# Kernel optimization log

Hardware: AMD Instinct MI355X
Metric: run time of the kernel (lower is better)

The kernel has to match this reference:

```python
import jax, jax.numpy as jnp
import numpy as np

SIZE = 48          # grid edge
DIST = 4           # local neighborhood edge
PAD = DIST // 2    # padding = 2
PADDED = SIZE + 2 * PAD  # 52
RATE = 5           # recurrent steps
CONVEY = 0.9
N_IN = 2048        # input injection sites


def setup_inputs() -> dict:
    key = jax.random.key(0)
    ks = jax.random.split(key, 8)
    neuron_matrix = jnp.zeros((PADDED, PADDED, PADDED), dtype=jnp.float32)
    vinput = jax.random.normal(ks[0], (N_IN,), dtype=jnp.float32)
    # scale synapse so the 5-step relu recurrence stays numerically tame
    synapse = jax.random.normal(ks[1], (SIZE, SIZE, SIZE, DIST, DIST, DIST), dtype=jnp.float32) * 0.05
    W1 = jax.random.normal(ks[2], (SIZE ** 3, 1024), dtype=jnp.float32) * (1.0 / np.sqrt(SIZE ** 3))
    b1 = jnp.zeros((1024,), dtype=jnp.float32)
    W2 = jax.random.normal(ks[3], (1024, 128), dtype=jnp.float32) * (1.0 / np.sqrt(1024))
    b2 = jnp.zeros((128,), dtype=jnp.float32)
    W3 = jax.random.normal(ks[4], (128, 10), dtype=jnp.float32) * (1.0 / np.sqrt(128))
    b3 = jnp.zeros((10,), dtype=jnp.float32)
    node_idx = jax.random.randint(ks[5], (N_IN, 3), 0, SIZE)  # interior coords
    return {"neuron_matrix": neuron_matrix, "vinput": vinput, "synapse": synapse,
            "W1": W1, "b1": b1, "W2": W2, "b2": b2, "W3": W3, "b3": b3,
            "node_idx": node_idx}


def _windows(p):
    # p: [PADDED]^3 -> sliding DxDxD windows at every interior site: [S,S,S,D,D,D]
    idx = jnp.arange(SIZE)[:, None] + jnp.arange(DIST)[None, :]  # [S, D]
    w = jnp.take(p, idx, axis=0)   # [S, D, P, P]
    w = jnp.take(w, idx, axis=2)   # [S, D, S, D, P]
    w = jnp.take(w, idx, axis=4)   # [S, D, S, D, S, D]
    return jnp.transpose(w, (0, 2, 4, 1, 3, 5))  # [S, S, S, D, D, D]


def reference(neuron_matrix, vinput, synapse, W1, b1, W2, b2, W3, b3, node_idx):
    # inject inputs at (possibly colliding) interior nodes (scatter-add, like +=)
    nm = neuron_matrix.at[node_idx[:, 0] + PAD,
                          node_idx[:, 1] + PAD,
                          node_idx[:, 2] + PAD].add(vinput)
    # recurrent locally-connected 3D neighbor aggregation, RATE steps
    for _ in range(RATE):
        win = _windows(nm)  # [S,S,S,D,D,D]
        agg = jnp.einsum('xyzabc,xyzabc->xyz', synapse, win)  # per-site unique-weight reduce
        interior = jax.nn.relu(agg) * CONVEY
        nm = jnp.pad(interior, PAD)  # re-pad with zeros for next step
    x = interior.reshape(1, SIZE ** 3)
    x = jax.nn.relu(x @ W1 + b1)
    x = jax.nn.relu(x @ W2 + b2)
    return x @ W3 + b3  # [1, 10]
```

## Files before the change

### kernel.cpp

```cpp
#include <hip/hip_runtime.h>

#define S 48
#define D 4
#define PADC 2
#define P 52
#define SITES (S * S * S)
#define PADVOL (P * P * P)
#define N_IN 2048
#define H1 1024
#define H2 128
#define OUTN 10
#define RP 64
#define NCH (SITES / RP)
#define RG 16
#define CHPG (NCH / RG)
#define G2B 32

__global__ void scatter_k(const float* __restrict__ vin,
                          const int* __restrict__ idx,
                          float* __restrict__ nm) {
    int t = blockIdx.x * blockDim.x + threadIdx.x;
    if (t < N_IN) {
        int x = idx[t * 3 + 0] + PADC;
        int y = idx[t * 3 + 1] + PADC;
        int z = idx[t * 3 + 2] + PADC;
        atomicAdd(&nm[(x * P + y) * P + z], vin[t]);
    }
}

__global__ __launch_bounds__(256) void step_k(const float* __restrict__ src,
                                              const float* __restrict__ syn,
                                              float* __restrict__ dst) {
    int tid = threadIdx.x;
    int half = tid & 1;
    int sl = tid >> 1;
    int s = blockIdx.x * 128 + sl;
    int z = s % S;
    int q = s / S;
    int y = q % S;
    int x = q / S;
    const float4* sv = (const float4*)(syn + (size_t)s * 64) + half * 8;
    int a0 = half * 2;
    float acc = 0.0f;
#pragma unroll
    for (int a = 0; a < 2; a++) {
#pragma unroll
        for (int b = 0; b < D; b++) {
            const float* row = src + ((x + a0 + a) * P + (y + b)) * P + z;
            float4 w = sv[a * 4 + b];
            acc += w.x * row[0] + w.y * row[1] + w.z * row[2] + w.w * row[3];
        }
    }
    acc += __shfl_xor(acc, 1);
    if (half == 0) {
        acc = fmaxf(acc, 0.0f) * 0.9f;
        dst[((x + PADC) * P + (y + PADC)) * P + (z + PADC)] = acc;
    }
}

__global__ __launch_bounds__(256) void gemv1_k(const float* __restrict__ nmfin,
                                               const float* __restrict__ W1,
                                               float* __restrict__ partial) {
    __shared__ float xs[RP];
    int t = threadIdx.x;
    int lane = t & 63;
    int i0 = blockIdx.x * RP;

    int i = i0 + lane;
    int z = i % S;
    int q = i / S;
    int y = q % S;
    int x = q / S;
    float v = nmfin[((x + PADC) * P + (y + PADC)) * P + (z + PADC)];
    unsigned long long mask = __ballot(v != 0.0f);
    if (t < RP) xs[t] = v;
    __syncthreads();

    const float4* W4 = (const float4*)W1;
    size_t base = (size_t)i0 * (H1 / 4) + t;
    float4 a0 = {0.f, 0.f, 0.f, 0.f};
    float4 a1 = {0.f, 0.f, 0.f, 0.f};
    while (mask) {
        int r0 = (int)__builtin_ctzll(mask);
        mask &= mask - 1;
        if (mask) {
            int r1 = (int)__builtin_ctzll(mask);
            mask &= mask - 1;
            float x0 = xs[r0], x1 = xs[r1];
            float4 w0 = W4[base + (size_t)r0 * (H1 / 4)];
            float4 w1 = W4[base + (size_t)r1 * (H1 / 4)];
            a0.x += x0 * w0.x; a0.y += x0 * w0.y; a0.z += x0 * w0.z; a0.w += x0 * w0.w;
            a1.x += x1 * w1.x; a1.y += x1 * w1.y; a1.z += x1 * w1.z; a1.w += x1 * w1.w;
        } else {
            float x0 = xs[r0];
            float4 w0 = W4[base + (size_t)r0 * (H1 / 4)];
            a0.x += x0 * w0.x; a0.y += x0 * w0.y; a0.z += x0 * w0.z; a0.w += x0 * w0.w;
        }
    }
    float4 acc = {a0.x + a1.x, a0.y + a1.y, a0.z + a1.z, a0.w + a1.w};
    ((float4*)(partial + (size_t)blockIdx.x * H1))[t] = acc;
}

__global__ __launch_bounds__(256) void reduceA_k(const float* __restrict__ partial,
                                                 float* __restrict__ redB) {
    int g = blockIdx.x >> 2;
    int c = (blockIdx.x & 3) * 256 + threadIdx.x;
    float s = 0.0f;
    int r0 = g * CHPG;
#pragma unroll 4
    for (int r = r0; r < r0 + CHPG; r++) s += partial[(size_t)r * H1 + c];
    redB[g * H1 + c] = s;
}

__global__ __launch_bounds__(128) void gemv2_k(const float* __restrict__ redB,
                                               const float* __restrict__ b1,
                                               const float* __restrict__ W2,
                                               float* __restrict__ partial2) {
    __shared__ float ys[H1 / G2B];
    int b = blockIdx.x;
    int t = threadIdx.x;
    int r0 = b * (H1 / G2B);
    if (t < H1 / G2B) {
        int j = r0 + t;
        float s = b1[j];
#pragma unroll
        for (int g = 0; g < RG; g++) s += redB[g * H1 + j];
        ys[t] = fmaxf(s, 0.0f);
    }
    __syncthreads();
    float acc = 0.0f;
#pragma unroll
    for (int i = 0; i < H1 / G2B; i++)
        acc += ys[i] * W2[(size_t)(r0 + i) * H2 + t];
    partial2[b * H2 + t] = acc;
}

__global__ __launch_bounds__(128) void final_k(const float* __restrict__ partial2,
                                               const float* __restrict__ b2,
                                               const float* __restrict__ W3,
                                               const float* __restrict__ b3,
                                               float* __restrict__ out) {
    __shared__ float y2[H2];
    int t = threadIdx.x;
    float s = b2[t];
#pragma unroll
    for (int k = 0; k < G2B; k++) s += partial2[k * H2 + t];
    y2[t] = fmaxf(s, 0.0f);
    __syncthreads();
    if (t < OUTN) {
        float o = b3[t];
#pragma unroll 8
        for (int i = 0; i < H2; i++) o += y2[i] * W3[i * OUTN + t];
        out[t] = o;
    }
}

extern "C" void kernel_launch(void* const* d_in, const int* in_sizes, int n_in,
                              void* d_out, int out_size, void* d_ws, size_t ws_size,
                              hipStream_t stream) {
    const float* vinput  = (const float*)d_in[1];
    const float* synapse = (const float*)d_in[2];
    const float* W1      = (const float*)d_in[3];
    const float* b1      = (const float*)d_in[4];
    const float* W2      = (const float*)d_in[5];
    const float* b2      = (const float*)d_in[6];
    const float* W3      = (const float*)d_in[7];
    const float* b3      = (const float*)d_in[8];
    const int* node_idx  = (const int*)d_in[9];

    float* ws = (float*)d_ws;
    float* nm0 = ws;
    float* nm1 = nm0 + PADVOL;
    float* partial1 = nm1 + PADVOL;
    float* redB = partial1 + (size_t)NCH * H1;
    float* partial2 = redB + RG * H1;
    float* out = (float*)d_out;

    hipMemsetAsync(nm0, 0, 2 * (size_t)PADVOL * sizeof(float), stream);

    scatter_k<<<N_IN / 256, 256, 0, stream>>>(vinput, node_idx, nm0);

    const float* src = nm0;
    float* dst = nm1;
    for (int r = 0; r < 5; r++) {
        step_k<<<SITES / 128, 256, 0, stream>>>(src, synapse, dst);
        float* tmp = (float*)src;
        src = dst;
        dst = tmp;
    }

    gemv1_k<<<NCH, 256, 0, stream>>>(src, W1, partial1);
    reduceA_k<<<RG * 4, 256, 0, stream>>>(partial1, redB);
    gemv2_k<<<G2B, 128, 0, stream>>>(redB, b1, W2, partial2);
    final_k<<<1, 128, 0, stream>>>(partial2, b2, W3, b3, out);
}
```

Baseline: 107.3 us.

## Split stencil site across four lanes and replace memset with zero kernel

Each stencil site in the recurrent step is now handled by four threads, one per y-offset, instead of two. The threads combine their partial sums with two xor shuffles, and the grid doubles to 64 sites per block. This gives more parallelism and shorter per-thread dependency chains for the bandwidth-bound synapse read, at the cost of an extra shuffle and lower per-thread work. The hipMemsetAsync of the two padded buffers is also replaced by a custom float4 zeroing kernel, likely to cut memset launch overhead.

```diff
diff --git a/kernel.cpp b/kernel.cpp
--- a/kernel.cpp
+++ b/kernel.cpp
@@ -16,6 +16,11 @@
 #define CHPG (NCH / RG)
 #define G2B 32
 
+__global__ __launch_bounds__(256) void zero_k(float4* __restrict__ p, int n4) {
+    int i = blockIdx.x * 256 + threadIdx.x;
+    if (i < n4) p[i] = make_float4(0.f, 0.f, 0.f, 0.f);
+}
+
 __global__ void scatter_k(const float* __restrict__ vin,
                           const int* __restrict__ idx,
                           float* __restrict__ nm) {
@@ -32,29 +37,25 @@
                                               const float* __restrict__ syn,
                                               float* __restrict__ dst) {
     int tid = threadIdx.x;
-    int half = tid & 1;
-    int sl = tid >> 1;
-    int s = blockIdx.x * 128 + sl;
+    int q = tid & 3;
+    int sl = tid >> 2;
+    int s = blockIdx.x * 64 + sl;
     int z = s % S;
-    int q = s / S;
-    int y = q % S;
-    int x = q / S;
-    const float4* sv = (const float4*)(syn + (size_t)s * 64) + half * 8;
-    int a0 = half * 2;
+    int t2 = s / S;
+    int y = t2 % S;
+    int x = t2 / S;
+    const float4* sv = (const float4*)(syn + (size_t)s * 64);
     float acc = 0.0f;
 #pragma unroll
-    for (int a = 0; a < 2; a++) {
-#pragma unroll
-        for (int b = 0; b < D; b++) {
-            const float* row = src + ((x + a0 + a) * P + (y + b)) * P + z;
-            float4 w = sv[a * 4 + b];
-            acc += w.x * row[0] + w.y * row[1] + w.z * row[2] + w.w * row[3];
-        }
+    for (int a = 0; a < D; a++) {
+        const float* row = src + ((x + a) * P + (y + q)) * P + z;
+        float4 w = sv[a * 4 + q];
+        acc += w.x * row[0] + w.y * row[1] + w.z * row[2] + w.w * row[3];
     }
     acc += __shfl_xor(acc, 1);
-    if (half == 0) {
-        acc = fmaxf(acc, 0.0f) * 0.9f;
-        dst[((x + PADC) * P + (y + PADC)) * P + (z + PADC)] = acc;
+    acc += __shfl_xor(acc, 2);
+    if (q == 0) {
+        dst[((x + PADC) * P + (y + PADC)) * P + (z + PADC)] = fmaxf(acc, 0.0f) * 0.9f;
     }
 }
 
@@ -176,14 +177,15 @@
     float* partial2 = redB + RG * H1;
     float* out = (float*)d_out;
 
-    hipMemsetAsync(nm0, 0, 2 * (size_t)PADVOL * sizeof(float), stream);
+    const int n4 = 2 * PADVOL / 4;
+    zero_k<<<(n4 + 255) / 256, 256, 0, stream>>>((float4*)nm0, n4);
 
     scatter_k<<<N_IN / 256, 256, 0, stream>>>(vinput, node_idx, nm0);
 
     const float* src = nm0;
     float* dst = nm1;
     for (int r = 0; r < 5; r++) {
-        step_k<<<SITES / 128, 256, 0, stream>>>(src, synapse, dst);
+        step_k<<<SITES / 64, 256, 0, stream>>>(src, synapse, dst);
         float* tmp = (float*)src;
         src = dst;
         dst = tmp;
```

New measurement: 93.50 us. 12.8% less time.
